# Kernel optimization log

Measured on AMD Instinct MI355X. Metric: run time of the kernel, lower is better.

Reference implementation:

```python
import jax, jax.numpy as jnp
import numpy as np

N = 50000      # nodes
E = 800000     # edges (before self-loops)
IN = 256
HID = 256
OUT = 128
D = 4
K = 4
K1 = 8
NUM_KS = K1 * ((1 << K) - 1)   # 120 centroids
S = HID // D                   # sub-dim per quantization slice
TAU = 1.0


def setup_inputs() -> dict:
    key = jax.random.key(0)
    ks = jax.random.split(key, 9)
    x = jax.random.normal(ks[0], (N, IN), jnp.float32)
    edge_index = jax.random.randint(ks[1], (2, E), 0, N, dtype=jnp.int64)
    def lin(k, fan_in, fan_out):
        return jax.random.normal(k, (fan_in, fan_out), jnp.float32) / np.float32(np.sqrt(fan_in))
    W0 = lin(ks[2], IN, HID); b0 = jnp.zeros((HID,), jnp.float32)
    W1 = lin(ks[3], HID, HID); b1 = jnp.zeros((HID,), jnp.float32)
    W2 = lin(ks[4], HID, OUT); b2 = jnp.zeros((OUT,), jnp.float32)
    # kaiming_normal on (NUM_KS, HID): std = sqrt(2 / fan_in), fan_in = HID
    centroids = jax.random.normal(ks[5], (NUM_KS, HID), jnp.float32) * np.float32(np.sqrt(2.0 / HID))
    return dict(x=x, edge_index=edge_index, W0=W0, b0=b0, W1=W1, b1=b1, W2=W2, b2=b2,
                centroids=centroids)


def gcn_conv(x, W, b, src, dst):
    # PyG GCNConv: add self-loops, symmetric normalization, aggregate at target
    n = x.shape[0]
    loops = jnp.arange(n, dtype=src.dtype)
    s2 = jnp.concatenate([src, loops])
    d2 = jnp.concatenate([dst, loops])
    deg = jax.ops.segment_sum(jnp.ones_like(d2, x.dtype), d2, num_segments=n)
    dinv = jnp.where(deg > 0, jax.lax.rsqrt(deg), 0.0)
    norm = dinv[s2] * dinv[d2]                      # [E+n]
    xw = x @ W                                      # [n, out]
    out = jax.ops.segment_sum(xw[s2] * norm[:, None], d2, num_segments=n)
    return out + b


def quantize(H, C):
    # H: [n, HID], C: [NUM_KS, HID]
    n = H.shape[0]
    Hr = H.reshape(n, D, S)
    Cr = C.reshape(NUM_KS, D, S)
    # products[n,k,d] = sum_s H[n,d,s] * C[k,d,s]
    prods = jnp.einsum('nds,kds->nkd', Hr, Cr) / TAU   # [n, NUM_KS, D]
    soft_l, hard_l, prob_l = [], [], []
    off = 0
    d_idx = jnp.arange(D)[None, :]
    for j in range(K):                 # K fixed small groups of sizes k_1<<j
        m = K1 << j
        sl = prods[:, off:off + m, :]                  # [n, m, D]
        p = jax.nn.softmax(sl, axis=1)                 # scatter_softmax within group
        Cg = Cr[off:off + m]                           # [m, D, S]
        soft_l.append(jnp.einsum('nmd,mds->nds', p, Cg))
        idx = jnp.argmax(sl, axis=1)                   # [n, D] scatter_max within group
        hard_l.append(Cg[idx, d_idx, :])               # [n, D, S]
        prob_l.append(p)
        off += m
    soft = jnp.stack(soft_l, 1).reshape(n, K, HID)
    hard = jnp.stack(hard_l, 1).reshape(n, K, HID)
    q = jax.lax.stop_gradient(hard - soft) + soft      # straight-through
    balance = jnp.concatenate(prob_l, 1).sum(0) / n    # [NUM_KS, D]
    k_blns = jnp.concatenate([jnp.full((K1 << j,), 1.0 / (K1 << j), jnp.float32) for j in range(K)])
    target = jnp.broadcast_to(k_blns[:, None], (NUM_KS, D))
    reg = jnp.linalg.norm(balance - target)
    pred = jnp.max(q, axis=1)                          # [n, HID]
    return pred, reg


def reference(x, edge_index, W0, b0, W1, b1, W2, b2, centroids):
    src, dst = edge_index[0], edge_index[1]
    h = jax.nn.leaky_relu(gcn_conv(x, W0, b0, src, dst), negative_slope=0.5)
    h = jax.nn.leaky_relu(gcn_conv(h, W1, b1, src, dst), negative_slope=0.5)
    pred, reg = quantize(h, centroids)
    h = h + pred
    out = gcn_conv(h, W2, b2, src, dst)
    return out, reg
```

## Files before the change

kernel.cpp:

```cpp
#include <hip/hip_runtime.h>
#include <math.h>


typedef short bf16x8 __attribute__((ext_vector_type(8)));
typedef float f32x4 __attribute__((ext_vector_type(4)));

__device__ __forceinline__ unsigned short bf16_rne(float a) {
    unsigned u = __builtin_bit_cast(unsigned, a);
    return (unsigned short)((u + 0x7FFFu + ((u >> 16) & 1u)) >> 16);
}
__device__ __forceinline__ float bf16_to_f(unsigned short h) {
    return __builtin_bit_cast(float, (unsigned)h << 16);
}
__device__ __forceinline__ void split4(const float* e, unsigned short* h, unsigned short* l) {
#pragma unroll
    for (int t = 0; t < 4; ++t) {
        h[t] = bf16_rne(e[t]);
        l[t] = bf16_rne(e[t] - bf16_to_f(h[t]));
    }
}


__global__ void k_init(int* cnt, int* cursor, int* counter, float* balance, int n) {
    int i = blockIdx.x * blockDim.x + threadIdx.x;
    if (i < n) { cnt[i] = 0; cursor[i] = 0; }
    if (i < 480) balance[i] = 0.f;
    if (i == 0) *counter = 0;
}

__global__ void k_count(const int* __restrict__ dst, int* __restrict__ cnt, int e) {
    int i = blockIdx.x * blockDim.x + threadIdx.x;
    if (i < e) atomicAdd(&cnt[dst[i]], 1);
}

__global__ void k_allocdinv(const int* __restrict__ cnt, int* __restrict__ row_start,
                            int* __restrict__ counter, float* __restrict__ dinv, int n) {
    int i = blockIdx.x * blockDim.x + threadIdx.x;
    if (i < n) {
        row_start[i] = atomicAdd(counter, cnt[i]);
        dinv[i] = rsqrtf((float)cnt[i] + 1.0f);
    }
}

__global__ void k_fill(const int* __restrict__ src, const int* __restrict__ dst,
                       const float* __restrict__ dinv, const int* __restrict__ row_start,
                       int* __restrict__ cursor, int* __restrict__ csr_src,
                       float* __restrict__ csr_norm, int e) {
    int i = blockIdx.x * blockDim.x + threadIdx.x;
    if (i >= e) return;
    int s = src[i], d = dst[i];
    int slot = atomicAdd(&cursor[d], 1);
    int idx = row_start[d] + slot;
    csr_src[idx] = s;
    csr_norm[idx] = dinv[s] * dinv[d];
}


__global__ void k_splitW3(const float* __restrict__ W0, const float* __restrict__ W1,
                          const float* __restrict__ W2,
                          short* __restrict__ w0h, short* __restrict__ w0l,
                          short* __restrict__ w1h, short* __restrict__ w1l,
                          short* __restrict__ w2h, short* __restrict__ w2l) {
    int i = blockIdx.x * blockDim.x + threadIdx.x;
    if (i >= 163840) return;
    float v;
    short *ph, *pl;
    int j;
    if (i < 65536) {
        j = i; v = W0[(j & 255) * 256 + (j >> 8)]; ph = w0h; pl = w0l;
    } else if (i < 131072) {
        j = i - 65536; v = W1[(j & 255) * 256 + (j >> 8)]; ph = w1h; pl = w1l;
    } else {
        j = i - 131072; v = W2[(j & 255) * 128 + (j >> 8)]; ph = w2h; pl = w2l;
    }
    unsigned short h = bf16_rne(v);
    ph[j] = (short)h;
    pl[j] = (short)bf16_rne(v - bf16_to_f(h));
}

__global__ void k_splitA(const float* __restrict__ X, short* __restrict__ Hi,
                         short* __restrict__ Lo, int total8) {
    int i = blockIdx.x * blockDim.x + threadIdx.x;
    if (i >= total8) return;
    float4 a = *(const float4*)(X + (size_t)i * 8);
    float4 b = *(const float4*)(X + (size_t)i * 8 + 4);
    float e0[4] = {a.x, a.y, a.z, a.w}, e1[4] = {b.x, b.y, b.z, b.w};
    unsigned short h0[4], l0[4], h1[4], l1[4];
    split4(e0, h0, l0);
    split4(e1, h1, l1);
    *(uint4*)(Hi + (size_t)i * 8) = make_uint4(h0[0] | (h0[1] << 16), h0[2] | (h0[3] << 16),
                                              h1[0] | (h1[1] << 16), h1[2] | (h1[3] << 16));
    *(uint4*)(Lo + (size_t)i * 8) = make_uint4(l0[0] | (l0[1] << 16), l0[2] | (l0[3] << 16),
                                              l1[0] | (l1[1] << 16), l1[2] | (l1[3] << 16));
}


__global__ __launch_bounds__(256, 2) void k_gemm_bf16s(const short* __restrict__ Ah,
                                                       const short* __restrict__ Al,
                                                       const short* __restrict__ Bh,
                                                       const short* __restrict__ Bl,
                                                       float* __restrict__ C,
                                                       int M, int N) {
    __shared__ short smem[4 * 128 * 56];
    short* Ash = smem;
    short* Asl = smem + 7168;
    short* Bsh = smem + 14336;
    short* Bsl = smem + 21504;
    const int tid = threadIdx.x;
    const int bm = blockIdx.x * 128;
    const int bn = blockIdx.y * 128;
    const int wave = tid >> 6, lane = tid & 63;
    const int wr = wave >> 1, wc = wave & 1;
    const int lr = lane & 15, lk = lane >> 4;

    int srow[2], ssg[2];
    bool aval[2];
#pragma unroll
    for (int it = 0; it < 2; ++it) {
        int u = it * 256 + tid;
        srow[it] = u >> 2;
        ssg[it] = (u & 3) << 3;
        aval[it] = (bm + srow[it]) < M;
    }

    const bf16x8 z8 = {0, 0, 0, 0, 0, 0, 0, 0};
    bf16x8 pah[2], pal[2], pbh[2], pbl[2];

    auto prefetch = [&](int k0) {
#pragma unroll
        for (int it = 0; it < 2; ++it) {
            size_t arow = (size_t)(bm + srow[it]) * 256 + k0 + ssg[it];
            size_t brow = (size_t)(bn + srow[it]) * 256 + k0 + ssg[it];
            pah[it] = aval[it] ? *(const bf16x8*)(Ah + arow) : z8;
            pal[it] = aval[it] ? *(const bf16x8*)(Al + arow) : z8;
            pbh[it] = *(const bf16x8*)(Bh + brow);
            pbl[it] = *(const bf16x8*)(Bl + brow);
        }
    };

    f32x4 acc[4][4] = {};
    prefetch(0);

    for (int k0 = 0; k0 < 256; k0 += 32) {
#pragma unroll
        for (int it = 0; it < 2; ++it) {
            int off = srow[it] * 56 + ssg[it];
            *(bf16x8*)&Ash[off] = pah[it];
            *(bf16x8*)&Asl[off] = pal[it];
            *(bf16x8*)&Bsh[off] = pbh[it];
            *(bf16x8*)&Bsl[off] = pbl[it];
        }
        __syncthreads();

        bf16x8 ah[4], al[4], bh[4], bl[4];
#pragma unroll
        for (int i = 0; i < 4; ++i) {
            int off = (wr * 64 + i * 16 + lr) * 56 + lk * 8;
            ah[i] = *(bf16x8*)&Ash[off];
            al[i] = *(bf16x8*)&Asl[off];
        }
#pragma unroll
        for (int j = 0; j < 4; ++j) {
            int off = (wc * 64 + j * 16 + lr) * 56 + lk * 8;
            bh[j] = *(bf16x8*)&Bsh[off];
            bl[j] = *(bf16x8*)&Bsl[off];
        }

        if (k0 < 224) prefetch(k0 + 32);

#pragma unroll
        for (int i = 0; i < 4; ++i)
#pragma unroll
            for (int j = 0; j < 4; ++j) {
                acc[i][j] = __builtin_amdgcn_mfma_f32_16x16x32_bf16(al[i], bh[j], acc[i][j], 0, 0, 0);
                acc[i][j] = __builtin_amdgcn_mfma_f32_16x16x32_bf16(ah[i], bl[j], acc[i][j], 0, 0, 0);
                acc[i][j] = __builtin_amdgcn_mfma_f32_16x16x32_bf16(ah[i], bh[j], acc[i][j], 0, 0, 0);
            }
        __syncthreads();
    }

    float* Cs = (float*)smem;
#pragma unroll
    for (int p = 0; p < 2; ++p) {
        if (wc == p) {
#pragma unroll
            for (int i = 0; i < 4; ++i)
#pragma unroll
                for (int r = 0; r < 4; ++r) {
                    int row = wr * 64 + i * 16 + lk * 4 + r;
#pragma unroll
                    for (int j = 0; j < 4; ++j)
                        Cs[row * 68 + j * 16 + lr] = acc[i][j][r];
                }
        }
        __syncthreads();
#pragma unroll
        for (int t = 0; t < 8; ++t) {
            int idx = t * 256 + tid;
            int row = idx >> 4, c4 = idx & 15;
            if (bm + row < M)
                *(float4*)(C + (size_t)(bm + row) * N + bn + p * 64 + c4 * 4) =
                    *(const float4*)&Cs[row * 68 + c4 * 4];
        }
        __syncthreads();
    }
}


template <bool RELU, int MODE>
__global__ __launch_bounds__(256, 4) void k_agg4(const float* __restrict__ xw,
                                                 const float* __restrict__ dinv,
                                                 const int* __restrict__ csr_src,
                                                 const float* __restrict__ csr_norm,
                                                 const int* __restrict__ row_start,
                                                 const int* __restrict__ cnt,
                                                 const float* __restrict__ bias,
                                                 float* __restrict__ out,
                                                 short* __restrict__ outH,
                                                 short* __restrict__ outL, int n) {
    int node = blockIdx.x * 4 + (threadIdx.x >> 6);
    if (node >= n) return;
    int lane = threadIdx.x & 63;
    int c = lane * 4;
    float di = dinv[node];
    float4 self = *(const float4*)(xw + (size_t)node * 256 + c);
    float4 bv = *(const float4*)(bias + c);
    float sw = di * di;
    float ax = self.x * sw + bv.x;
    float ay = self.y * sw + bv.y;
    float az = self.z * sw + bv.z;
    float aw = self.w * sw + bv.w;
    int st = row_start[node];
    int m = cnt[node];
    for (int t0 = 0; t0 < m; t0 += 64) {
        int rem = m - t0;
        int cnt_i = rem < 64 ? rem : 64;
        int idx_l = 0;
        float nrm_l = 0.f;
        if (lane < cnt_i) {
            idx_l = csr_src[st + t0 + lane];
            nrm_l = csr_norm[st + t0 + lane];
        }
        int t = 0;
        for (; t + 8 <= cnt_i; t += 8) {
            const float* p0 = xw + (size_t)__shfl(idx_l, t + 0, 64) * 256 + c;
            const float* p1 = xw + (size_t)__shfl(idx_l, t + 1, 64) * 256 + c;
            const float* p2 = xw + (size_t)__shfl(idx_l, t + 2, 64) * 256 + c;
            const float* p3 = xw + (size_t)__shfl(idx_l, t + 3, 64) * 256 + c;
            const float* p4 = xw + (size_t)__shfl(idx_l, t + 4, 64) * 256 + c;
            const float* p5 = xw + (size_t)__shfl(idx_l, t + 5, 64) * 256 + c;
            const float* p6 = xw + (size_t)__shfl(idx_l, t + 6, 64) * 256 + c;
            const float* p7 = xw + (size_t)__shfl(idx_l, t + 7, 64) * 256 + c;
            float4 v0 = *(const float4*)p0;
            float4 v1 = *(const float4*)p1;
            float4 v2 = *(const float4*)p2;
            float4 v3 = *(const float4*)p3;
            float4 v4 = *(const float4*)p4;
            float4 v5 = *(const float4*)p5;
            float4 v6 = *(const float4*)p6;
            float4 v7 = *(const float4*)p7;
            float w0 = __shfl(nrm_l, t + 0, 64);
            float w1 = __shfl(nrm_l, t + 1, 64);
            float w2 = __shfl(nrm_l, t + 2, 64);
            float w3 = __shfl(nrm_l, t + 3, 64);
            float w4 = __shfl(nrm_l, t + 4, 64);
            float w5 = __shfl(nrm_l, t + 5, 64);
            float w6 = __shfl(nrm_l, t + 6, 64);
            float w7 = __shfl(nrm_l, t + 7, 64);
            ax += v0.x * w0; ay += v0.y * w0; az += v0.z * w0; aw += v0.w * w0;
            ax += v1.x * w1; ay += v1.y * w1; az += v1.z * w1; aw += v1.w * w1;
            ax += v2.x * w2; ay += v2.y * w2; az += v2.z * w2; aw += v2.w * w2;
            ax += v3.x * w3; ay += v3.y * w3; az += v3.z * w3; aw += v3.w * w3;
            ax += v4.x * w4; ay += v4.y * w4; az += v4.z * w4; aw += v4.w * w4;
            ax += v5.x * w5; ay += v5.y * w5; az += v5.z * w5; aw += v5.w * w5;
            ax += v6.x * w6; ay += v6.y * w6; az += v6.z * w6; aw += v6.w * w6;
            ax += v7.x * w7; ay += v7.y * w7; az += v7.z * w7; aw += v7.w * w7;
        }
        for (; t < cnt_i; ++t) {
            int s = __shfl(idx_l, t, 64);
            float w = __shfl(nrm_l, t, 64);
            float4 v = *(const float4*)(xw + (size_t)s * 256 + c);
            ax += v.x * w; ay += v.y * w; az += v.z * w; aw += v.w * w;
        }
    }
    if (RELU) {
        ax = ax > 0.f ? ax : 0.5f * ax;
        ay = ay > 0.f ? ay : 0.5f * ay;
        az = az > 0.f ? az : 0.5f * az;
        aw = aw > 0.f ? aw : 0.5f * aw;
    }
    if (MODE == 0) {
        *(float4*)(out + (size_t)node * 256 + c) = make_float4(ax, ay, az, aw);
    } else {
        float e[4] = {ax, ay, az, aw};
        unsigned short h[4], l[4];
        split4(e, h, l);
        size_t o = (size_t)node * 256 + c;
        *(uint2*)(outH + o) = make_uint2(h[0] | (h[1] << 16), h[2] | (h[3] << 16));
        *(uint2*)(outL + o) = make_uint2(l[0] | (l[1] << 16), l[2] | (l[3] << 16));
    }
}

__global__ __launch_bounds__(256, 4) void k_agg2(const float* __restrict__ xw,
                                                 const float* __restrict__ dinv,
                                                 const int* __restrict__ csr_src,
                                                 const float* __restrict__ csr_norm,
                                                 const int* __restrict__ row_start,
                                                 const int* __restrict__ cnt,
                                                 const float* __restrict__ bias,
                                                 float* __restrict__ out, int n) {
    int node = blockIdx.x * 4 + (threadIdx.x >> 6);
    if (node >= n) return;
    int lane = threadIdx.x & 63;
    int c = lane * 2;
    float di = dinv[node];
    float2 self = *(const float2*)(xw + (size_t)node * 128 + c);
    float2 bv = *(const float2*)(bias + c);
    float sw = di * di;
    float ax = self.x * sw + bv.x;
    float ay = self.y * sw + bv.y;
    int st = row_start[node];
    int m = cnt[node];
    for (int t0 = 0; t0 < m; t0 += 64) {
        int rem = m - t0;
        int cnt_i = rem < 64 ? rem : 64;
        int idx_l = 0;
        float nrm_l = 0.f;
        if (lane < cnt_i) {
            idx_l = csr_src[st + t0 + lane];
            nrm_l = csr_norm[st + t0 + lane];
        }
        int t = 0;
        for (; t + 8 <= cnt_i; t += 8) {
            const float* p0 = xw + (size_t)__shfl(idx_l, t + 0, 64) * 128 + c;
            const float* p1 = xw + (size_t)__shfl(idx_l, t + 1, 64) * 128 + c;
            const float* p2 = xw + (size_t)__shfl(idx_l, t + 2, 64) * 128 + c;
            const float* p3 = xw + (size_t)__shfl(idx_l, t + 3, 64) * 128 + c;
            const float* p4 = xw + (size_t)__shfl(idx_l, t + 4, 64) * 128 + c;
            const float* p5 = xw + (size_t)__shfl(idx_l, t + 5, 64) * 128 + c;
            const float* p6 = xw + (size_t)__shfl(idx_l, t + 6, 64) * 128 + c;
            const float* p7 = xw + (size_t)__shfl(idx_l, t + 7, 64) * 128 + c;
            float2 v0 = *(const float2*)p0;
            float2 v1 = *(const float2*)p1;
            float2 v2 = *(const float2*)p2;
            float2 v3 = *(const float2*)p3;
            float2 v4 = *(const float2*)p4;
            float2 v5 = *(const float2*)p5;
            float2 v6 = *(const float2*)p6;
            float2 v7 = *(const float2*)p7;
            float w0 = __shfl(nrm_l, t + 0, 64);
            float w1 = __shfl(nrm_l, t + 1, 64);
            float w2 = __shfl(nrm_l, t + 2, 64);
            float w3 = __shfl(nrm_l, t + 3, 64);
            float w4 = __shfl(nrm_l, t + 4, 64);
            float w5 = __shfl(nrm_l, t + 5, 64);
            float w6 = __shfl(nrm_l, t + 6, 64);
            float w7 = __shfl(nrm_l, t + 7, 64);
            ax += v0.x * w0; ay += v0.y * w0;
            ax += v1.x * w1; ay += v1.y * w1;
            ax += v2.x * w2; ay += v2.y * w2;
            ax += v3.x * w3; ay += v3.y * w3;
            ax += v4.x * w4; ay += v4.y * w4;
            ax += v5.x * w5; ay += v5.y * w5;
            ax += v6.x * w6; ay += v6.y * w6;
            ax += v7.x * w7; ay += v7.y * w7;
        }
        for (; t < cnt_i; ++t) {
            int s = __shfl(idx_l, t, 64);
            float w = __shfl(nrm_l, t, 64);
            float2 v = *(const float2*)(xw + (size_t)s * 128 + c);
            ax += v.x * w; ay += v.y * w;
        }
    }
    *(float2*)(out + (size_t)node * 128 + c) = make_float2(ax, ay);
}


__global__ __launch_bounds__(256, 4) void k_quant4(const float* __restrict__ h2,
                                                   const float* __restrict__ cent,
                                                   short* __restrict__ h3h,
                                                   short* __restrict__ h3l,
                                                   float* __restrict__ balance_g, int n) {
    __shared__ float As[32 * 132];
    __shared__ float Bs[32 * 132];
    __shared__ float bal4[4 * 128];
    __shared__ int km_ls[128 * 4];
    const int tid = threadIdx.x;
    const int n0 = blockIdx.x * 128;
    const int d = blockIdx.y;
    const int ty = tid >> 4, tx = tid & 15;
    const int wave = tid >> 6, lane = tid & 63;

    int gid, base, sz;
    if (tx == 0)       { gid = 0; base = 0;  sz = 1; }
    else if (tx <= 2)  { gid = 1; base = 1;  sz = 2; }
    else if (tx <= 6)  { gid = 2; base = 3;  sz = 4; }
    else if (tx <= 14) { gid = 3; base = 7;  sz = 8; }
    else               { gid = 0; base = 15; sz = 0; }
    const int l = tx - base;
    const int segbase = lane & 48;

    {
        int k = tid >> 3, r = tid & 7;
        int col = (r < 4) ? (60 + r) : (120 + r);
        Bs[k * 132 + col] = 0.f;
    }

    const int srow = tid >> 3, sk4 = tid & 7;
    float acc[8][8] = {};

#pragma unroll
    for (int it = 0; it < 4; ++it) {
        int row = srow + it * 32;
        float4 v = make_float4(0.f, 0.f, 0.f, 0.f);
        if (n0 + row < n)
            v = *(const float4*)(h2 + (size_t)(n0 + row) * 256 + d * 64 + sk4 * 4);
        As[(sk4 * 4 + 0) * 132 + row] = v.x;
        As[(sk4 * 4 + 1) * 132 + row] = v.y;
        As[(sk4 * 4 + 2) * 132 + row] = v.z;
        As[(sk4 * 4 + 3) * 132 + row] = v.w;
    }
#pragma unroll
    for (int it = 0; it < 4; ++it) {
        int q = it * 256 + tid;
        if (q < 960) {
            int cc = q >> 3, k4 = q & 7;
            float4 v = *(const float4*)(cent + (size_t)cc * 256 + d * 64 + k4 * 4);
            int col = ((cc >> 3) << 2) + (((cc >> 2) & 1) << 6) + (cc & 3);
            Bs[(k4 * 4 + 0) * 132 + col] = v.x;
            Bs[(k4 * 4 + 1) * 132 + col] = v.y;
            Bs[(k4 * 4 + 2) * 132 + col] = v.z;
            Bs[(k4 * 4 + 3) * 132 + col] = v.w;
        }
    }
    float4 ph[4];
#pragma unroll
    for (int it = 0; it < 4; ++it) {
        int row = srow + it * 32;
        ph[it] = make_float4(0.f, 0.f, 0.f, 0.f);
        if (n0 + row < n)
            ph[it] = *(const float4*)(h2 + (size_t)(n0 + row) * 256 + d * 64 + 32 + sk4 * 4);
    }
    __syncthreads();

#pragma unroll 4
    for (int k = 0; k < 32; ++k) {
        float4 a0 = *(const float4*)&As[k * 132 + ty * 8];
        float4 a1 = *(const float4*)&As[k * 132 + ty * 8 + 4];
        float4 b0 = *(const float4*)&Bs[k * 132 + tx * 4];
        float4 b1 = *(const float4*)&Bs[k * 132 + 64 + tx * 4];
        float av[8] = {a0.x, a0.y, a0.z, a0.w, a1.x, a1.y, a1.z, a1.w};
        float bv[8] = {b0.x, b0.y, b0.z, b0.w, b1.x, b1.y, b1.z, b1.w};
#pragma unroll
        for (int i = 0; i < 8; ++i)
#pragma unroll
            for (int j = 0; j < 8; ++j)
                acc[i][j] += av[i] * bv[j];
    }
    __syncthreads();

#pragma unroll
    for (int it = 0; it < 4; ++it) {
        int row = srow + it * 32;
        As[(sk4 * 4 + 0) * 132 + row] = ph[it].x;
        As[(sk4 * 4 + 1) * 132 + row] = ph[it].y;
        As[(sk4 * 4 + 2) * 132 + row] = ph[it].z;
        As[(sk4 * 4 + 3) * 132 + row] = ph[it].w;
    }
#pragma unroll
    for (int it = 0; it < 4; ++it) {
        int q = it * 256 + tid;
        if (q < 960) {
            int cc = q >> 3, k4 = q & 7;
            float4 v = *(const float4*)(cent + (size_t)cc * 256 + d * 64 + 32 + k4 * 4);
            int col = ((cc >> 3) << 2) + (((cc >> 2) & 1) << 6) + (cc & 3);
            Bs[(k4 * 4 + 0) * 132 + col] = v.x;
            Bs[(k4 * 4 + 1) * 132 + col] = v.y;
            Bs[(k4 * 4 + 2) * 132 + col] = v.z;
            Bs[(k4 * 4 + 3) * 132 + col] = v.w;
        }
    }
    __syncthreads();

#pragma unroll 4
    for (int k = 0; k < 32; ++k) {
        float4 a0 = *(const float4*)&As[k * 132 + ty * 8];
        float4 a1 = *(const float4*)&As[k * 132 + ty * 8 + 4];
        float4 b0 = *(const float4*)&Bs[k * 132 + tx * 4];
        float4 b1 = *(const float4*)&Bs[k * 132 + 64 + tx * 4];
        float av[8] = {a0.x, a0.y, a0.z, a0.w, a1.x, a1.y, a1.z, a1.w};
        float bv[8] = {b0.x, b0.y, b0.z, b0.w, b1.x, b1.y, b1.z, b1.w};
#pragma unroll
        for (int i = 0; i < 8; ++i)
#pragma unroll
            for (int j = 0; j < 8; ++j)
                acc[i][j] += av[i] * bv[j];
    }

    float balp[8] = {};
#pragma unroll
    for (int i = 0; i < 8; ++i) {
        const int node = ty * 8 + i;
        const bool act = (n0 + node) < n;
        float m = acc[i][0];
        int am = tx * 8;
#pragma unroll
        for (int j = 1; j < 8; ++j)
            if (acc[i][j] > m) { m = acc[i][j]; am = tx * 8 + j; }
#pragma unroll
        for (int s = 1; s <= 4; s <<= 1) {
            int pl = l ^ s;
            int srcl = segbase + base + pl;
            float mo = __shfl(m, srcl, 64);
            int amo = __shfl(am, srcl, 64);
            if (pl < sz && (mo > m || (mo == m && amo < am))) { m = mo; am = amo; }
        }
        float Z = 0.f;
#pragma unroll
        for (int j = 0; j < 8; ++j) {
            float e2 = expf(acc[i][j] - m);
            acc[i][j] = e2;
            Z += e2;
        }
#pragma unroll
        for (int s = 1; s <= 4; s <<= 1) {
            int pl = l ^ s;
            int srcl = segbase + base + pl;
            float Zo = __shfl(Z, srcl, 64);
            if (pl < sz) Z += Zo;
        }
        float invZ = (act && sz > 0) ? (1.0f / Z) : 0.f;
#pragma unroll
        for (int j = 0; j < 8; ++j) balp[j] += acc[i][j] * invZ;
        if (l == 0 && sz > 0) km_ls[node * 4 + gid] = am;
    }

#pragma unroll
    for (int j = 0; j < 8; ++j) {
        float v = balp[j];
        v += __shfl_xor(v, 16, 64);
        v += __shfl_xor(v, 32, 64);
        balp[j] = v;
    }
    if (lane < 16) {
#pragma unroll
        for (int j = 0; j < 8; ++j)
            bal4[wave * 128 + tx * 8 + j] = balp[j];
    }
    __syncthreads();
    if (tid < 120) {
        float s = bal4[tid] + bal4[128 + tid] + bal4[256 + tid] + bal4[384 + tid];
        atomicAdd(&balance_g[tid * 4 + d], s);
    }

    {
        const int node = tid >> 1;
        const int half = tid & 1;
        if (n0 + node < n) {
            int k0 = km_ls[node * 4 + 0], k1 = km_ls[node * 4 + 1];
            int k2 = km_ls[node * 4 + 2], k3 = km_ls[node * 4 + 3];
            const float* hp = h2 + (size_t)(n0 + node) * 256 + d * 64 + half * 32;
            const float* c0 = cent + (size_t)k0 * 256 + d * 64 + half * 32;
            const float* c1 = cent + (size_t)k1 * 256 + d * 64 + half * 32;
            const float* c2 = cent + (size_t)k2 * 256 + d * 64 + half * 32;
            const float* c3 = cent + (size_t)k3 * 256 + d * 64 + half * 32;
            size_t obase = (size_t)(n0 + node) * 256 + d * 64 + half * 32;
#pragma unroll
            for (int q = 0; q < 8; ++q) {
                int g = q * 4;
                float4 hv = *(const float4*)(hp + g);
                float4 v0 = *(const float4*)(c0 + g);
                float4 v1 = *(const float4*)(c1 + g);
                float4 v2 = *(const float4*)(c2 + g);
                float4 v3 = *(const float4*)(c3 + g);
                float e[4];
                e[0] = hv.x + fmaxf(fmaxf(v0.x, v1.x), fmaxf(v2.x, v3.x));
                e[1] = hv.y + fmaxf(fmaxf(v0.y, v1.y), fmaxf(v2.y, v3.y));
                e[2] = hv.z + fmaxf(fmaxf(v0.z, v1.z), fmaxf(v2.z, v3.z));
                e[3] = hv.w + fmaxf(fmaxf(v0.w, v1.w), fmaxf(v2.w, v3.w));
                unsigned short h[4], l[4];
                split4(e, h, l);
                *(uint2*)(h3h + obase + g) = make_uint2(h[0] | (h[1] << 16), h[2] | (h[3] << 16));
                *(uint2*)(h3l + obase + g) = make_uint2(l[0] | (l[1] << 16), l[2] | (l[3] << 16));
            }
        }
    }
}

__global__ void k_reg(const float* __restrict__ balance_g, float* __restrict__ out_reg,
                      float inv_n) {
    __shared__ float red[512];
    int tid = threadIdx.x;
    float v = 0.f;
    if (tid < 480) {
        int k = tid >> 2;
        float target = (k < 8) ? 0.125f : (k < 24) ? 0.0625f : (k < 56) ? 0.03125f : 0.015625f;
        float b = balance_g[tid] * inv_n;
        float df = b - target;
        v = df * df;
    }
    red[tid] = v;
    __syncthreads();
    for (int s = 256; s > 0; s >>= 1) {
        if (tid < s) red[tid] += red[tid + s];
        __syncthreads();
    }
    if (tid == 0) *out_reg = sqrtf(red[0]);
}


extern "C" void kernel_launch(void* const* d_in, const int* in_sizes, int n_in,
                              void* d_out, int out_size, void* d_ws, size_t ws_size,
                              hipStream_t stream) {
    const float* x    = (const float*)d_in[0];
    const int*   ei   = (const int*)d_in[1];
    const float* W0   = (const float*)d_in[2];
    const float* b0   = (const float*)d_in[3];
    const float* W1   = (const float*)d_in[4];
    const float* b1   = (const float*)d_in[5];
    const float* W2   = (const float*)d_in[6];
    const float* b2   = (const float*)d_in[7];
    const float* cent = (const float*)d_in[8];
    const int n = in_sizes[0] / 256;
    const int e = in_sizes[1] / 2;
    const int* src = ei;
    const int* dst = ei + e;
    float* out = (float*)d_out;

    char* w = (char*)d_ws;
    float* bufA = (float*)w;      w += (size_t)n * 256 * 4;
    float* bufB = (float*)w;      w += (size_t)n * 256 * 4;
    float* dinv = (float*)w;      w += (size_t)n * 4;
    int* cnt = (int*)w;           w += (size_t)n * 4;
    int* row_start = (int*)w;     w += (size_t)n * 4;
    int* cursor = (int*)w;        w += (size_t)n * 4;
    int* csr_src = (int*)w;       w += (size_t)e * 4;
    float* csr_norm = (float*)w;  w += (size_t)e * 4;
    int* counter = (int*)w;       w += 256;
    float* balance = (float*)w;   w += 480 * 4;
    short* w0h = (short*)w;       w += 256 * 256 * 2;
    short* w0l = (short*)w;       w += 256 * 256 * 2;
    short* w1h = (short*)w;       w += 256 * 256 * 2;
    short* w1l = (short*)w;       w += 256 * 256 * 2;
    short* w2h = (short*)w;       w += 128 * 256 * 2;
    short* w2l = (short*)w;       w += 128 * 256 * 2;

    short* xh = (short*)bufA;
    short* xl = xh + (size_t)n * 256;
    short* h1h = (short*)bufA;
    short* h1l = h1h + (size_t)n * 256;
    short* h3h = (short*)bufB;
    short* h3l = h3h + (size_t)n * 256;

    const int tb = 256;
    k_init<<<(n + tb - 1) / tb, tb, 0, stream>>>(cnt, cursor, counter, balance, n);
    k_count<<<(e + tb - 1) / tb, tb, 0, stream>>>(dst, cnt, e);
    k_allocdinv<<<(n + tb - 1) / tb, tb, 0, stream>>>(cnt, row_start, counter, dinv, n);
    k_fill<<<(e + tb - 1) / tb, tb, 0, stream>>>(src, dst, dinv, row_start, cursor,
                                                 csr_src, csr_norm, e);

    k_splitW3<<<(163840 + tb - 1) / tb, tb, 0, stream>>>(W0, W1, W2, w0h, w0l,
                                                         w1h, w1l, w2h, w2l);
    k_splitA<<<(n * 32 + tb - 1) / tb, tb, 0, stream>>>(x, xh, xl, n * 32);

    dim3 g1((n + 127) / 128, 2);
    k_gemm_bf16s<<<g1, 256, 0, stream>>>(xh, xl, w0h, w0l, bufB, n, 256);
    k_agg4<true, 1><<<(n + 3) / 4, 256, 0, stream>>>(bufB, dinv, csr_src, csr_norm,
                                                     row_start, cnt, b0, nullptr,
                                                     h1h, h1l, n);
    k_gemm_bf16s<<<g1, 256, 0, stream>>>(h1h, h1l, w1h, w1l, bufB, n, 256);
    k_agg4<true, 0><<<(n + 3) / 4, 256, 0, stream>>>(bufB, dinv, csr_src, csr_norm,
                                                     row_start, cnt, b1, bufA,
                                                     nullptr, nullptr, n);

    dim3 gq((n + 127) / 128, 4);
    k_quant4<<<gq, 256, 0, stream>>>(bufA, cent, h3h, h3l, balance, n);

    dim3 g3((n + 127) / 128, 1);
    k_gemm_bf16s<<<g3, 256, 0, stream>>>(h3h, h3l, w2h, w2l, bufA, n, 128);
    k_agg2<<<(n + 3) / 4, 256, 0, stream>>>(bufA, dinv, csr_src, csr_norm,
                                            row_start, cnt, b2, out, n);
    k_reg<<<1, 512, 0, stream>>>(balance, out + (size_t)n * 128, 1.0f / (float)n);
}
```

Before: 608.3 us.

## Move quantization scores to split-bf16 MFMA and emit bf16 hi/lo from aggregation

Replaces the FP32 SIMT outer-product GEMM in the quantizer with split-bf16 (hi/lo, three-product) MFMA 16x16x32 instructions. Centroids are pre-split into padded bf16 hi/lo buffers alongside the weights. The second aggregation now writes bf16 hi/lo halves directly instead of fp32, which halves the bytes the quantizer reads and lets it rebuild h from shared memory. The risks are slight numeric differences from the split-bf16 approximation, which could flip argmax ties, and lower occupancy from the new launch bounds.

Measured after the change: 640.9 us. 5.4% more time.

```diff
diff --git a/kernel.cpp b/kernel.cpp
--- a/kernel.cpp
+++ b/kernel.cpp
@@ -56,13 +56,13 @@
 }
 
 
-__global__ void k_splitW3(const float* __restrict__ W0, const float* __restrict__ W1,
-                          const float* __restrict__ W2,
+__global__ void k_splitWC(const float* __restrict__ W0, const float* __restrict__ W1,
+                          const float* __restrict__ W2, const float* __restrict__ cent,
                           short* __restrict__ w0h, short* __restrict__ w0l,
                           short* __restrict__ w1h, short* __restrict__ w1l,
-                          short* __restrict__ w2h, short* __restrict__ w2l) {
+                          short* __restrict__ w2h, short* __restrict__ w2l,
+                          short* __restrict__ ch, short* __restrict__ cl) {
     int i = blockIdx.x * blockDim.x + threadIdx.x;
-    if (i >= 163840) return;
     float v;
     short *ph, *pl;
     int j;
@@ -70,8 +70,11 @@
         j = i; v = W0[(j & 255) * 256 + (j >> 8)]; ph = w0h; pl = w0l;
     } else if (i < 131072) {
         j = i - 65536; v = W1[(j & 255) * 256 + (j >> 8)]; ph = w1h; pl = w1l;
+    } else if (i < 163840) {
+        j = i - 131072; v = W2[(j & 255) * 128 + (j >> 8)]; ph = w2h; pl = w2l;
     } else {
-        j = i - 131072; v = W2[(j & 255) * 128 + (j >> 8)]; ph = w2h; pl = w2l;
+        j = i - 163840; int c = j >> 8;
+        v = (c < 120) ? cent[j] : 0.f; ph = ch; pl = cl;
     }
     unsigned short h = bf16_rne(v);
     ph[j] = (short)h;
@@ -376,177 +379,170 @@
 }
 
 
-__global__ __launch_bounds__(256, 4) void k_quant4(const float* __restrict__ h2,
+#define SM_UPD1(AV, MG, AG, CB, R)                                      \
+    { float vv = AV[R]; int cid = (CB) + lk4 + (R);                     \
+      if (vv > MG) { MG = vv; AG = cid; } }
+#define SM_UPD(AV, MG, AG, CB)                                          \
+    SM_UPD1(AV, MG, AG, CB, 0) SM_UPD1(AV, MG, AG, CB, 1)               \
+    SM_UPD1(AV, MG, AG, CB, 2) SM_UPD1(AV, MG, AG, CB, 3)
+#define SM_BFLY(MG, AG)                                                 \
+    { float mo = __shfl_xor(MG, 16, 64); int ao = __shfl_xor(AG, 16, 64); \
+      if (mo > MG || (mo == MG && ao < AG)) { MG = mo; AG = ao; }       \
+      mo = __shfl_xor(MG, 32, 64); ao = __shfl_xor(AG, 32, 64);         \
+      if (mo > MG || (mo == MG && ao < AG)) { MG = mo; AG = ao; } }
+#define SM_EXPZ1(AV, MG, ZG, R)                                         \
+    { float e2 = expf(AV[R] - MG); AV[R] = e2; ZG += e2; }
+#define SM_EXPZ(AV, MG, ZG)                                             \
+    SM_EXPZ1(AV, MG, ZG, 0) SM_EXPZ1(AV, MG, ZG, 1)                     \
+    SM_EXPZ1(AV, MG, ZG, 2) SM_EXPZ1(AV, MG, ZG, 3)
+#define SM_ZBF(ZG) { ZG += __shfl_xor(ZG, 16, 64); ZG += __shfl_xor(ZG, 32, 64); }
+#define SM_BAL1(AV, IZ, BP, R) { BP[R] += AV[R] * (IZ); }
+#define SM_BAL(AV, IZ, BP)                                              \
+    SM_BAL1(AV, IZ, BP, 0) SM_BAL1(AV, IZ, BP, 1)                       \
+    SM_BAL1(AV, IZ, BP, 2) SM_BAL1(AV, IZ, BP, 3)
+
+#define Q9_SM(A0, A1, A2, A3, A4, A5, A6, A7, NODE)                     \
+    {                                                                   \
+        const int node_ = (NODE);                                       \
+        const bool act_ = (n0 + node_) < n;                             \
+        float mg0 = -3.4e38f, mg1 = -3.4e38f, mg2 = -3.4e38f, mg3 = -3.4e38f; \
+        int ag0 = 0x7FFFFFFF, ag1 = 0x7FFFFFFF, ag2 = 0x7FFFFFFF, ag3 = 0x7FFFFFFF; \
+        if (lkh == 0) {                                                 \
+            SM_UPD(A0, mg0, ag0, 0)   SM_UPD(A1, mg1, ag1, 16)          \
+            SM_UPD(A2, mg2, ag2, 32)  SM_UPD(A3, mg2, ag2, 48)          \
+            SM_UPD(A4, mg3, ag3, 64)  SM_UPD(A5, mg3, ag3, 80)          \
+            SM_UPD(A6, mg3, ag3, 96)  SM_UPD(A7, mg3, ag3, 112)         \
+        } else {                                                        \
+            SM_UPD(A0, mg1, ag1, 0)                                     \
+            SM_UPD(A1, mg2, ag2, 16)  SM_UPD(A2, mg2, ag2, 32)          \
+            SM_UPD(A3, mg3, ag3, 48)  SM_UPD(A4, mg3, ag3, 64)          \
+            SM_UPD(A5, mg3, ag3, 80)  SM_UPD(A6, mg3, ag3, 96)          \
+        }                                                               \
+        SM_BFLY(mg0, ag0) SM_BFLY(mg1, ag1) SM_BFLY(mg2, ag2) SM_BFLY(mg3, ag3) \
+        float zg0 = 0.f, zg1 = 0.f, zg2 = 0.f, zg3 = 0.f;               \
+        if (lkh == 0) {                                                 \
+            SM_EXPZ(A0, mg0, zg0) SM_EXPZ(A1, mg1, zg1)                 \
+            SM_EXPZ(A2, mg2, zg2) SM_EXPZ(A3, mg2, zg2)                 \
+            SM_EXPZ(A4, mg3, zg3) SM_EXPZ(A5, mg3, zg3)                 \
+            SM_EXPZ(A6, mg3, zg3) SM_EXPZ(A7, mg3, zg3)                 \
+        } else {                                                        \
+            SM_EXPZ(A0, mg1, zg1)                                       \
+            SM_EXPZ(A1, mg2, zg2) SM_EXPZ(A2, mg2, zg2)                 \
+            SM_EXPZ(A3, mg3, zg3) SM_EXPZ(A4, mg3, zg3)                 \
+            SM_EXPZ(A5, mg3, zg3) SM_EXPZ(A6, mg3, zg3)                 \
+        }                                                               \
+        SM_ZBF(zg0) SM_ZBF(zg1) SM_ZBF(zg2) SM_ZBF(zg3)                 \
+        float iz0 = act_ ? (1.0f / zg0) : 0.f;                          \
+        float iz1 = act_ ? (1.0f / zg1) : 0.f;                          \
+        float iz2 = act_ ? (1.0f / zg2) : 0.f;                          \
+        float iz3 = act_ ? (1.0f / zg3) : 0.f;                          \
+        if (lkh == 0) {                                                 \
+            SM_BAL(A0, iz0, balp0) SM_BAL(A1, iz1, balp1)               \
+            SM_BAL(A2, iz2, balp2) SM_BAL(A3, iz2, balp3)               \
+            SM_BAL(A4, iz3, balp4) SM_BAL(A5, iz3, balp5)               \
+            SM_BAL(A6, iz3, balp6) SM_BAL(A7, iz3, balp7)               \
+        } else {                                                        \
+            SM_BAL(A0, iz1, balp0)                                      \
+            SM_BAL(A1, iz2, balp1) SM_BAL(A2, iz2, balp2)               \
+            SM_BAL(A3, iz3, balp3) SM_BAL(A4, iz3, balp4)               \
+            SM_BAL(A5, iz3, balp5) SM_BAL(A6, iz3, balp6)               \
+        }                                                               \
+        if (lk == 0) {                                                  \
+            km_ls[node_ * 4 + 0] = ag0; km_ls[node_ * 4 + 1] = ag1;     \
+            km_ls[node_ * 4 + 2] = ag2; km_ls[node_ * 4 + 3] = ag3;     \
+        }                                                               \
+    }
+
+#define Q9_MFMA(AV, CT, NH, NL)                                         \
+    { size_t boff_ = (size_t)((CT) * 16 + l) * 256 + d * 64 + kc * 32 + lk * 8; \
+      bf16x8 cbh_ = *(const bf16x8*)(ch + boff_);                       \
+      bf16x8 cbl_ = *(const bf16x8*)(cl + boff_);                       \
+      AV = __builtin_amdgcn_mfma_f32_16x16x32_bf16(cbl_, NH, AV, 0, 0, 0); \
+      AV = __builtin_amdgcn_mfma_f32_16x16x32_bf16(cbh_, NL, AV, 0, 0, 0); \
+      AV = __builtin_amdgcn_mfma_f32_16x16x32_bf16(cbh_, NH, AV, 0, 0, 0); }
+
+__global__ __launch_bounds__(256, 3) void k_quant9(const short* __restrict__ h2h,
+                                                   const short* __restrict__ h2l,
+                                                   const short* __restrict__ ch,
+                                                   const short* __restrict__ cl,
                                                    const float* __restrict__ cent,
                                                    short* __restrict__ h3h,
                                                    short* __restrict__ h3l,
                                                    float* __restrict__ balance_g, int n) {
-    __shared__ float As[32 * 132];
-    __shared__ float Bs[32 * 132];
+    __shared__ short Ah[128 * 72];
+    __shared__ short Al[128 * 72];
     __shared__ float bal4[4 * 128];
     __shared__ int km_ls[128 * 4];
     const int tid = threadIdx.x;
     const int n0 = blockIdx.x * 128;
     const int d = blockIdx.y;
-    const int ty = tid >> 4, tx = tid & 15;
     const int wave = tid >> 6, lane = tid & 63;
-
-    int gid, base, sz;
-    if (tx == 0)       { gid = 0; base = 0;  sz = 1; }
-    else if (tx <= 2)  { gid = 1; base = 1;  sz = 2; }
-    else if (tx <= 6)  { gid = 2; base = 3;  sz = 4; }
-    else if (tx <= 14) { gid = 3; base = 7;  sz = 8; }
-    else               { gid = 0; base = 15; sz = 0; }
-    const int l = tx - base;
-    const int segbase = lane & 48;
+    const int l = lane & 15, lk = lane >> 4;
+    const int lk4 = lk * 4;
+    const int lkh = lk >> 1;
 
     {
-        int k = tid >> 3, r = tid & 7;
-        int col = (r < 4) ? (60 + r) : (120 + r);
-        Bs[k * 132 + col] = 0.f;
-    }
-
-    const int srow = tid >> 3, sk4 = tid & 7;
-    float acc[8][8] = {};
-
-#pragma unroll
-    for (int it = 0; it < 4; ++it) {
-        int row = srow + it * 32;
-        float4 v = make_float4(0.f, 0.f, 0.f, 0.f);
-        if (n0 + row < n)
-            v = *(const float4*)(h2 + (size_t)(n0 + row) * 256 + d * 64 + sk4 * 4);
-        As[(sk4 * 4 + 0) * 132 + row] = v.x;
-        As[(sk4 * 4 + 1) * 132 + row] = v.y;
-        As[(sk4 * 4 + 2) * 132 + row] = v.z;
-        As[(sk4 * 4 + 3) * 132 + row] = v.w;
-    }
-#pragma unroll
-    for (int it = 0; it < 4; ++it) {
-        int q = it * 256 + tid;
-        if (q < 960) {
-            int cc = q >> 3, k4 = q & 7;
-            float4 v = *(const float4*)(cent + (size_t)cc * 256 + d * 64 + k4 * 4);
-            int col = ((cc >> 3) << 2) + (((cc >> 2) & 1) << 6) + (cc & 3);
-            Bs[(k4 * 4 + 0) * 132 + col] = v.x;
-            Bs[(k4 * 4 + 1) * 132 + col] = v.y;
-            Bs[(k4 * 4 + 2) * 132 + col] = v.z;
-            Bs[(k4 * 4 + 3) * 132 + col] = v.w;
-        }
-    }
-    float4 ph[4];
-#pragma unroll
-    for (int it = 0; it < 4; ++it) {
-        int row = srow + it * 32;
-        ph[it] = make_float4(0.f, 0.f, 0.f, 0.f);
-        if (n0 + row < n)
-            ph[it] = *(const float4*)(h2 + (size_t)(n0 + row) * 256 + d * 64 + 32 + sk4 * 4);
+        const int row = tid >> 1, half = tid & 1;
+        const size_t g = (size_t)(n0 + row) * 256 + d * 64 + half * 32;
+        const int o = row * 72 + half * 32;
+        const bf16x8 z8 = {0, 0, 0, 0, 0, 0, 0, 0};
+        bool v = (n0 + row) < n;
+#pragma unroll
+        for (int s = 0; s < 4; ++s) {
+            *(bf16x8*)&Ah[o + s * 8] = v ? *(const bf16x8*)(h2h + g + s * 8) : z8;
+            *(bf16x8*)&Al[o + s * 8] = v ? *(const bf16x8*)(h2l + g + s * 8) : z8;
+        }
     }
     __syncthreads();
 
-#pragma unroll 4
-    for (int k = 0; k < 32; ++k) {
-        float4 a0 = *(const float4*)&As[k * 132 + ty * 8];
-        float4 a1 = *(const float4*)&As[k * 132 + ty * 8 + 4];
-        float4 b0 = *(const float4*)&Bs[k * 132 + tx * 4];
-        float4 b1 = *(const float4*)&Bs[k * 132 + 64 + tx * 4];
-        float av[8] = {a0.x, a0.y, a0.z, a0.w, a1.x, a1.y, a1.z, a1.w};
-        float bv[8] = {b0.x, b0.y, b0.z, b0.w, b1.x, b1.y, b1.z, b1.w};
-#pragma unroll
-        for (int i = 0; i < 8; ++i)
-#pragma unroll
-            for (int j = 0; j < 8; ++j)
-                acc[i][j] += av[i] * bv[j];
-    }
-    __syncthreads();
-
-#pragma unroll
-    for (int it = 0; it < 4; ++it) {
-        int row = srow + it * 32;
-        As[(sk4 * 4 + 0) * 132 + row] = ph[it].x;
-        As[(sk4 * 4 + 1) * 132 + row] = ph[it].y;
-        As[(sk4 * 4 + 2) * 132 + row] = ph[it].z;
-        As[(sk4 * 4 + 3) * 132 + row] = ph[it].w;
-    }
-#pragma unroll
-    for (int it = 0; it < 4; ++it) {
-        int q = it * 256 + tid;
-        if (q < 960) {
-            int cc = q >> 3, k4 = q & 7;
-            float4 v = *(const float4*)(cent + (size_t)cc * 256 + d * 64 + 32 + k4 * 4);
-            int col = ((cc >> 3) << 2) + (((cc >> 2) & 1) << 6) + (cc & 3);
-            Bs[(k4 * 4 + 0) * 132 + col] = v.x;
-            Bs[(k4 * 4 + 1) * 132 + col] = v.y;
-            Bs[(k4 * 4 + 2) * 132 + col] = v.z;
-            Bs[(k4 * 4 + 3) * 132 + col] = v.w;
-        }
-    }
-    __syncthreads();
-
-#pragma unroll 4
-    for (int k = 0; k < 32; ++k) {
-        float4 a0 = *(const float4*)&As[k * 132 + ty * 8];
-        float4 a1 = *(const float4*)&As[k * 132 + ty * 8 + 4];
-        float4 b0 = *(const float4*)&Bs[k * 132 + tx * 4];
-        float4 b1 = *(const float4*)&Bs[k * 132 + 64 + tx * 4];
-        float av[8] = {a0.x, a0.y, a0.z, a0.w, a1.x, a1.y, a1.z, a1.w};
-        float bv[8] = {b0.x, b0.y, b0.z, b0.w, b1.x, b1.y, b1.z, b1.w};
-#pragma unroll
-        for (int i = 0; i < 8; ++i)
-#pragma unroll
-            for (int j = 0; j < 8; ++j)
-                acc[i][j] += av[i] * bv[j];
-    }
-
-    float balp[8] = {};
-#pragma unroll
-    for (int i = 0; i < 8; ++i) {
-        const int node = ty * 8 + i;
-        const bool act = (n0 + node) < n;
-        float m = acc[i][0];
-        int am = tx * 8;
-#pragma unroll
-        for (int j = 1; j < 8; ++j)
-            if (acc[i][j] > m) { m = acc[i][j]; am = tx * 8 + j; }
-#pragma unroll
-        for (int s = 1; s <= 4; s <<= 1) {
-            int pl = l ^ s;
-            int srcl = segbase + base + pl;
-            float mo = __shfl(m, srcl, 64);
-            int amo = __shfl(am, srcl, 64);
-            if (pl < sz && (mo > m || (mo == m && amo < am))) { m = mo; am = amo; }
-        }
-        float Z = 0.f;
-#pragma unroll
-        for (int j = 0; j < 8; ++j) {
-            float e2 = expf(acc[i][j] - m);
-            acc[i][j] = e2;
-            Z += e2;
-        }
-#pragma unroll
-        for (int s = 1; s <= 4; s <<= 1) {
-            int pl = l ^ s;
-            int srcl = segbase + base + pl;
-            float Zo = __shfl(Z, srcl, 64);
-            if (pl < sz) Z += Zo;
-        }
-        float invZ = (act && sz > 0) ? (1.0f / Z) : 0.f;
-#pragma unroll
-        for (int j = 0; j < 8; ++j) balp[j] += acc[i][j] * invZ;
-        if (l == 0 && sz > 0) km_ls[node * 4 + gid] = am;
-    }
-
-#pragma unroll
-    for (int j = 0; j < 8; ++j) {
-        float v = balp[j];
-        v += __shfl_xor(v, 16, 64);
-        v += __shfl_xor(v, 32, 64);
-        balp[j] = v;
-    }
-    if (lane < 16) {
-#pragma unroll
-        for (int j = 0; j < 8; ++j)
-            bal4[wave * 128 + tx * 8 + j] = balp[j];
-    }
+    f32x4 balp0 = {0.f, 0.f, 0.f, 0.f}, balp1 = {0.f, 0.f, 0.f, 0.f};
+    f32x4 balp2 = {0.f, 0.f, 0.f, 0.f}, balp3 = {0.f, 0.f, 0.f, 0.f};
+    f32x4 balp4 = {0.f, 0.f, 0.f, 0.f}, balp5 = {0.f, 0.f, 0.f, 0.f};
+    f32x4 balp6 = {0.f, 0.f, 0.f, 0.f}, balp7 = {0.f, 0.f, 0.f, 0.f};
+
+    {
+        f32x4 q0 = {0.f, 0.f, 0.f, 0.f}, q1 = {0.f, 0.f, 0.f, 0.f};
+        f32x4 q2 = {0.f, 0.f, 0.f, 0.f}, q3 = {0.f, 0.f, 0.f, 0.f};
+        f32x4 q4 = {0.f, 0.f, 0.f, 0.f}, q5 = {0.f, 0.f, 0.f, 0.f};
+        f32x4 q6 = {0.f, 0.f, 0.f, 0.f}, q7 = {0.f, 0.f, 0.f, 0.f};
+#pragma unroll
+        for (int kc = 0; kc < 2; ++kc) {
+            const int off = (wave * 32 + l) * 72 + kc * 32 + lk * 8;
+            bf16x8 nh = *(const bf16x8*)&Ah[off];
+            bf16x8 nl_ = *(const bf16x8*)&Al[off];
+            Q9_MFMA(q0, 0, nh, nl_) Q9_MFMA(q1, 1, nh, nl_)
+            Q9_MFMA(q2, 2, nh, nl_) Q9_MFMA(q3, 3, nh, nl_)
+            Q9_MFMA(q4, 4, nh, nl_) Q9_MFMA(q5, 5, nh, nl_)
+            Q9_MFMA(q6, 6, nh, nl_) Q9_MFMA(q7, 7, nh, nl_)
+        }
+        Q9_SM(q0, q1, q2, q3, q4, q5, q6, q7, wave * 32 + l)
+    }
+    {
+        f32x4 q0 = {0.f, 0.f, 0.f, 0.f}, q1 = {0.f, 0.f, 0.f, 0.f};
+        f32x4 q2 = {0.f, 0.f, 0.f, 0.f}, q3 = {0.f, 0.f, 0.f, 0.f};
+        f32x4 q4 = {0.f, 0.f, 0.f, 0.f}, q5 = {0.f, 0.f, 0.f, 0.f};
+        f32x4 q6 = {0.f, 0.f, 0.f, 0.f}, q7 = {0.f, 0.f, 0.f, 0.f};
+#pragma unroll
+        for (int kc = 0; kc < 2; ++kc) {
+            const int off = (wave * 32 + 16 + l) * 72 + kc * 32 + lk * 8;
+            bf16x8 nh = *(const bf16x8*)&Ah[off];
+            bf16x8 nl_ = *(const bf16x8*)&Al[off];
+            Q9_MFMA(q0, 0, nh, nl_) Q9_MFMA(q1, 1, nh, nl_)
+            Q9_MFMA(q2, 2, nh, nl_) Q9_MFMA(q3, 3, nh, nl_)
+            Q9_MFMA(q4, 4, nh, nl_) Q9_MFMA(q5, 5, nh, nl_)
+            Q9_MFMA(q6, 6, nh, nl_) Q9_MFMA(q7, 7, nh, nl_)
+        }
+        Q9_SM(q0, q1, q2, q3, q4, q5, q6, q7, wave * 32 + 16 + l)
+    }
+
+#define SM_BR1(BP, CB, R)                                               \
+    { float bb = BP[R];                                                 \
+      bb += __shfl_xor(bb, 1, 64); bb += __shfl_xor(bb, 2, 64);         \
+      bb += __shfl_xor(bb, 4, 64); bb += __shfl_xor(bb, 8, 64);         \
+      if (l == 0) bal4[wave * 128 + (CB) + lk4 + (R)] = bb; }
+#define SM_BR(BP, CB) SM_BR1(BP, CB, 0) SM_BR1(BP, CB, 1) SM_BR1(BP, CB, 2) SM_BR1(BP, CB, 3)
+    SM_BR(balp0, 0)  SM_BR(balp1, 16) SM_BR(balp2, 32) SM_BR(balp3, 48)
+    SM_BR(balp4, 64) SM_BR(balp5, 80) SM_BR(balp6, 96) SM_BR(balp7, 112)
     __syncthreads();
     if (tid < 120) {
         float s = bal4[tid] + bal4[128 + tid] + bal4[256 + tid] + bal4[384 + tid];
@@ -559,29 +555,32 @@
         if (n0 + node < n) {
             int k0 = km_ls[node * 4 + 0], k1 = km_ls[node * 4 + 1];
             int k2 = km_ls[node * 4 + 2], k3 = km_ls[node * 4 + 3];
-            const float* hp = h2 + (size_t)(n0 + node) * 256 + d * 64 + half * 32;
             const float* c0 = cent + (size_t)k0 * 256 + d * 64 + half * 32;
             const float* c1 = cent + (size_t)k1 * 256 + d * 64 + half * 32;
             const float* c2 = cent + (size_t)k2 * 256 + d * 64 + half * 32;
             const float* c3 = cent + (size_t)k3 * 256 + d * 64 + half * 32;
+            const int ao = node * 72 + half * 32;
             size_t obase = (size_t)(n0 + node) * 256 + d * 64 + half * 32;
 #pragma unroll
             for (int q = 0; q < 8; ++q) {
                 int g = q * 4;
-                float4 hv = *(const float4*)(hp + g);
                 float4 v0 = *(const float4*)(c0 + g);
                 float4 v1 = *(const float4*)(c1 + g);
                 float4 v2 = *(const float4*)(c2 + g);
                 float4 v3 = *(const float4*)(c3 + g);
                 float e[4];
-                e[0] = hv.x + fmaxf(fmaxf(v0.x, v1.x), fmaxf(v2.x, v3.x));
-                e[1] = hv.y + fmaxf(fmaxf(v0.y, v1.y), fmaxf(v2.y, v3.y));
-                e[2] = hv.z + fmaxf(fmaxf(v0.z, v1.z), fmaxf(v2.z, v3.z));
-                e[3] = hv.w + fmaxf(fmaxf(v0.w, v1.w), fmaxf(v2.w, v3.w));
-                unsigned short h[4], l[4];
-                split4(e, h, l);
+#pragma unroll
+                for (int u = 0; u < 4; ++u) {
+                    float hv = bf16_to_f((unsigned short)Ah[ao + g + u]) +
+                               bf16_to_f((unsigned short)Al[ao + g + u]);
+                    float m0 = fmaxf(fmaxf(((const float*)&v0)[u], ((const float*)&v1)[u]),
+                                     fmaxf(((const float*)&v2)[u], ((const float*)&v3)[u]));
+                    e[u] = hv + m0;
+                }
+                unsigned short h[4], lo[4];
+                split4(e, h, lo);
                 *(uint2*)(h3h + obase + g) = make_uint2(h[0] | (h[1] << 16), h[2] | (h[3] << 16));
-                *(uint2*)(h3l + obase + g) = make_uint2(l[0] | (l[1] << 16), l[2] | (l[3] << 16));
+                *(uint2*)(h3l + obase + g) = make_uint2(lo[0] | (lo[1] << 16), lo[2] | (lo[3] << 16));
             }
         }
     }
@@ -644,11 +643,15 @@
     short* w1l = (short*)w;       w += 256 * 256 * 2;
     short* w2h = (short*)w;       w += 128 * 256 * 2;
     short* w2l = (short*)w;       w += 128 * 256 * 2;
+    short* ch  = (short*)w;       w += 128 * 256 * 2;
+    short* cl  = (short*)w;       w += 128 * 256 * 2;
 
     short* xh = (short*)bufA;
     short* xl = xh + (size_t)n * 256;
     short* h1h = (short*)bufA;
     short* h1l = h1h + (size_t)n * 256;
+    short* h2h = (short*)bufA;
+    short* h2l = h2h + (size_t)n * 256;
     short* h3h = (short*)bufB;
     short* h3l = h3h + (size_t)n * 256;
 
@@ -659,8 +662,8 @@
     k_fill<<<(e + tb - 1) / tb, tb, 0, stream>>>(src, dst, dinv, row_start, cursor,
                                                  csr_src, csr_norm, e);
 
-    k_splitW3<<<(163840 + tb - 1) / tb, tb, 0, stream>>>(W0, W1, W2, w0h, w0l,
-                                                         w1h, w1l, w2h, w2l);
+    k_splitWC<<<196608 / tb, tb, 0, stream>>>(W0, W1, W2, cent, w0h, w0l, w1h, w1l,
+                                              w2h, w2l, ch, cl);
     k_splitA<<<(n * 32 + tb - 1) / tb, tb, 0, stream>>>(x, xh, xl, n * 32);
 
     dim3 g1((n + 127) / 128, 2);
@@ -669,12 +672,12 @@
                                                      row_start, cnt, b0, nullptr,
                                                      h1h, h1l, n);
     k_gemm_bf16s<<<g1, 256, 0, stream>>>(h1h, h1l, w1h, w1l, bufB, n, 256);
-    k_agg4<true, 0><<<(n + 3) / 4, 256, 0, stream>>>(bufB, dinv, csr_src, csr_norm,
-                                                     row_start, cnt, b1, bufA,
-                                                     nullptr, nullptr, n);
+    k_agg4<true, 1><<<(n + 3) / 4, 256, 0, stream>>>(bufB, dinv, csr_src, csr_norm,
+                                                     row_start, cnt, b1, nullptr,
+                                                     h2h, h2l, n);
 
     dim3 gq((n + 127) / 128, 4);
-    k_quant4<<<gq, 256, 0, stream>>>(bufA, cent, h3h, h3l, balance, n);
+    k_quant9<<<gq, 256, 0, stream>>>(h2h, h2l, ch, cl, cent, h3h, h3l, balance, n);
 
     dim3 g3((n + 127) / 128, 1);
     k_gemm_bf16s<<<g3, 256, 0, stream>>>(h3h, h3l, w2h, w2l, bufA, n, 128);
```
